# Performance work log

Hardware: AMD Instinct MI355X
Metric: run time of the kernel (lower is better)

Reference implementation:

```python
import jax, jax.numpy as jnp
import numpy as np
from jax import lax

B, C, L, G = 2048, 9605, 20, 50
ALPHA, ALPHA1, ALPHA2, ALPHA3, ALPHA_OTHER = 0.5, 0.05, 2.0, 10.0, 0.5
NEG_INF = jnp.float32(-1e30)


def setup_inputs() -> dict:
    k0, k1, k2, k3 = jax.random.split(jax.random.key(0), 4)
    x = jax.random.normal(k0, (B, C), jnp.float32)
    # sparse multi-label targets (~10 positives/row) so at most ~1 whitelist group is active,
    # matching the original code's assert len(gt_whitelist_index) == 1
    y = (jax.random.uniform(k1, (B, C)) < 0.001).astype(jnp.int32)
    y_neg = (jax.random.uniform(k2, (B, C)) < 0.001).astype(jnp.int32)
    # L disjoint whitelist groups of G classes each (from mapping_dict in the original)
    idx = jax.random.permutation(k3, C)[: L * G].reshape(L, G)
    group_mask = jnp.zeros((L, C), bool).at[jnp.arange(L)[:, None], idx].set(True)
    return {"x": x, "y": y, "y_neg": y_neg, "group_mask": group_mask}


def _rank_loss(x1, x2, margin):
    # our_rank_loss: sigmoid(alpha3*(x2-x1+margin)), scaled by alpha2 when positive
    d = x2 - x1 + margin
    s = jax.nn.sigmoid(ALPHA3 * d)
    return jnp.where(d > 0, ALPHA2 * s, s)


def reference(x, y, y_neg, group_mask):
    xs = jax.nn.sigmoid(x)  # [B, C]
    gmf = group_mask.astype(jnp.float32)  # [L, C]

    # per-row max score inside each whitelist group -> [B, L]
    # lax.map over the L (=20) groups keeps peak memory at one [B, C] temp per step
    group_max = lax.map(
        lambda m: jnp.max(jnp.where(m, xs, NEG_INF), axis=-1), group_mask
    ).T  # [B, L]

    # find_gt_whitelist: group k active iff sum(y[group_k]) > 0
    active = jnp.einsum("bc,lc->bl", y.astype(jnp.float32), gmf) > 0
    active_neg = jnp.einsum("bc,lc->bl", y_neg.astype(jnp.float32), gmf) > 0
    has_gt = jnp.any(active, axis=-1)  # [B]
    g = jnp.argmax(active, axis=-1)  # first active group (original asserts exactly one)

    # top_k_thres = max(11th largest sigmoid score, alpha_other) in both branches
    thres = jnp.maximum(lax.top_k(xs, 11)[0][:, 10], ALPHA_OTHER)  # [B]

    # max over union of all whitelist classes (wl_indices)
    union_max = jnp.max(jnp.where(jnp.any(group_mask, 0)[None, :], xs, NEG_INF), -1)

    gt_max = jnp.take_along_axis(group_max, g[:, None], axis=1)[:, 0]  # [B]
    # incorrect_max: max(0, max over groups != g); incorrect_neg: max(0, max over neg-active groups)
    excl = jnp.where(jnp.arange(L)[None, :] == g[:, None], NEG_INF, group_max)
    incorrect_max = jnp.maximum(jnp.max(excl, -1), 0.0)
    incorrect_neg = jnp.maximum(jnp.max(jnp.where(active_neg, group_max, 0.0), -1), 0.0)

    # branch A: no gt whitelist group active
    case_a = (1 - ALPHA) * _rank_loss(thres, union_max, ALPHA1) + ALPHA * _rank_loss(
        thres, incorrect_neg, ALPHA1
    )
    # branch B: exactly one gt group g
    case_b = (
        _rank_loss(gt_max, thres, ALPHA1)
        + jnp.where(
            incorrect_max > 0, (1 - ALPHA) * _rank_loss(thres, incorrect_max, ALPHA1), 0.0
        )
        + jnp.where(
            incorrect_neg > 0,
            ALPHA * _rank_loss(thres, incorrect_neg, ALPHA1),
            ALPHA * _rank_loss(thres, incorrect_max, ALPHA1),
        )
    )
    return jnp.sum(jnp.where(has_gt, case_b, case_a))
```

## Files before the change

kernel.cpp:

```cpp
#include <hip/hip_runtime.h>
#include <stdint.h>

#define B_ROWS 2048
#define C_CLS  9605
#define L_GRP  20
#define GM_BYTES (L_GRP * C_CLS)
#define REPSTRIDE 9728
#define GID_REGION (4 * REPSTRIDE)
#define NEG_BIG -3.0e38f

typedef float f32x4 __attribute__((ext_vector_type(4)));
typedef unsigned u32x4 __attribute__((ext_vector_type(4)));

__device__ __forceinline__ float sigmoidf(float v) {
  return 1.0f / (1.0f + __expf(-v));
}

__device__ __forceinline__ float rank_loss(float x1, float x2) {
  float d = x2 - x1 + 0.05f;
  float s = 1.0f / (1.0f + __expf(-10.0f * d));
  return d > 0.0f ? 2.0f * s : s;
}

__device__ __forceinline__ unsigned fmap(float f) {
  unsigned u = __float_as_uint(f);
  return (u & 0x80000000u) ? ~u : (u | 0x80000000u);
}
__device__ __forceinline__ float funmap(unsigned m) {
  unsigned u = (m & 0x80000000u) ? (m ^ 0x80000000u) : ~m;
  return __uint_as_float(u);
}

__global__ __launch_bounds__(256) void build_gid_kernel(
    const void* __restrict__ gm, unsigned char* __restrict__ ws,
    float* __restrict__ out) {
  __shared__ int s_part[4];
  __shared__ int s_total;
  const int tid = threadIdx.x;
  const int c = blockIdx.x * 256 + tid;
  if (c == 0) out[0] = 0.0f;

  int local = 0;
  const uint4* gm16 = (const uint4*)gm;
  const int nvec = GM_BYTES / 16;
  for (int i = tid; i < nvec; i += 256) {
    uint4 w = gm16[i];
    unsigned a[4] = {w.x, w.y, w.z, w.w};
#pragma unroll
    for (int q = 0; q < 4; ++q) {
      local += ((a[q] & 0x000000FFu) != 0) + ((a[q] & 0x0000FF00u) != 0) +
               ((a[q] & 0x00FF0000u) != 0) + ((a[q] & 0xFF000000u) != 0);
    }
  }
  if (tid == 0) {
    unsigned a = ((const unsigned*)gm)[nvec * 4];
    local += ((a & 0x000000FFu) != 0) + ((a & 0x0000FF00u) != 0) +
             ((a & 0x00FF0000u) != 0) + ((a & 0xFF000000u) != 0);
  }
#pragma unroll
  for (int off = 32; off; off >>= 1) local += __shfl_xor(local, off);
  if ((tid & 63) == 0) s_part[tid >> 6] = local;
  __syncthreads();
  if (tid == 0) s_total = s_part[0] + s_part[1] + s_part[2] + s_part[3];
  __syncthreads();
  const bool is_byte = (s_total > 600);

  if (c >= C_CLS) return;
  unsigned char g = 0xFF;
  if (is_byte) {
    const unsigned char* m8 = (const unsigned char*)gm;
#pragma unroll
    for (int l = L_GRP - 1; l >= 0; --l)
      if (m8[l * C_CLS + c] != 0) g = (unsigned char)l;
  } else {
    const unsigned* m32 = (const unsigned*)gm;
#pragma unroll
    for (int l = L_GRP - 1; l >= 0; --l)
      if (m32[l * C_CLS + c] != 0u) g = (unsigned char)l;
  }
  unsigned char* base = ws + 64;
#pragma unroll
  for (int r = 0; r < 4; ++r) base[r * REPSTRIDE + r + c] = g;
}

__global__ __launch_bounds__(256, 8) void loss_kernel(
    const float* __restrict__ x, const int* __restrict__ y,
    const int* __restrict__ yn, const unsigned char* __restrict__ ws64,
    float* __restrict__ out) {
  __shared__ unsigned s_gmax[L_GRP];
  __shared__ unsigned s_act, s_actn;
  __shared__ float s_wtop[4 * 11];
  const int tid = threadIdx.x;
  const int lane = tid & 63;
  const int wave = tid >> 6;
  const int row = blockIdx.x;

  const size_t base = (size_t)row * C_CLS;
  const int mis = (int)(base & 3);
  const int peel = (4 - mis) & 3;
  const float* xr = x + base;
  const int* yr = y + base;
  const int* nr = yn + base;
  const unsigned char* gidc = ws64 + mis * REPSTRIDE + mis;

  if (tid < L_GRP) s_gmax[tid] = 0u;
  if (tid == 0) { s_act = 0u; s_actn = 0u; }
  __syncthreads();

  float t[11];
#pragma unroll
  for (int i = 0; i < 11; ++i) t[i] = 0.0f;
  unsigned actL = 0u, actnL = 0u;

  auto ins = [&](float v) {
    if (v > t[10]) {
      float a = v;
#pragma unroll
      for (int i = 0; i < 11; ++i) {
        float hi = fmaxf(t[i], a); a = fminf(t[i], a); t[i] = hi;
      }
    }
  };
  auto gmax_upd = [&](unsigned gk, float v) {
    unsigned fm = fmap(v);
    if (fm > s_gmax[gk]) atomicMax(&s_gmax[gk], fm);
  };
  auto edge = [&](int c) {
    float v = xr[c];
    ins(v);
    unsigned gk = gidc[c];
    if (gk < L_GRP) {
      gmax_upd(gk, v);
      unsigned bit = 1u << gk;
      if (yr[c] != 0) actL |= bit;
      if (nr[c] != 0) actnL |= bit;
    }
  };

  if (tid < peel) edge(tid);
  const int nvec = (C_CLS - peel) >> 2;
  const int tail0 = peel + (nvec << 2);
  if (tid < C_CLS - tail0) edge(tail0 + tid);

  const f32x4* x4 = (const f32x4*)(xr + peel);
  const u32x4* y4 = (const u32x4*)(yr + peel);
  const u32x4* n4 = (const u32x4*)(nr + peel);
  const unsigned* g4 = (const unsigned*)(gidc + peel);

  auto quad = [&](f32x4 xv, u32x4 yv, u32x4 nv, unsigned gw) {
    if (gw != 0xFFFFFFFFu) {
      unsigned g0 = gw & 0xFFu, g1 = (gw >> 8) & 0xFFu,
               g2 = (gw >> 16) & 0xFFu, g3 = gw >> 24;
      if (g0 < L_GRP) gmax_upd(g0, xv.x);
      if (g1 < L_GRP) gmax_upd(g1, xv.y);
      if (g2 < L_GRP) gmax_upd(g2, xv.z);
      if (g3 < L_GRP) gmax_upd(g3, xv.w);
    }
    if (yv.x | yv.y | yv.z | yv.w | nv.x | nv.y | nv.z | nv.w) {
      const unsigned yq[4] = {yv.x, yv.y, yv.z, yv.w};
      const unsigned nq[4] = {nv.x, nv.y, nv.z, nv.w};
      const unsigned gq[4] = {gw & 0xFFu, (gw >> 8) & 0xFFu,
                              (gw >> 16) & 0xFFu, gw >> 24};
#pragma unroll
      for (int q = 0; q < 4; ++q) {
        if ((yq[q] | nq[q]) && gq[q] < L_GRP) {
          unsigned bit = 1u << gq[q];
          if (yq[q]) actL |= bit;
          if (nq[q]) actnL |= bit;
        }
      }
    }
    float am = fmaxf(fmaxf(xv.x, xv.y), fmaxf(xv.z, xv.w));
    if (am > t[10]) { ins(xv.x); ins(xv.y); ins(xv.z); ins(xv.w); }
  };

  int j = tid;
  for (; j + 256 < nvec; j += 512) {
    f32x4 xa = __builtin_nontemporal_load(x4 + j);
    f32x4 xb = __builtin_nontemporal_load(x4 + j + 256);
    u32x4 ya = __builtin_nontemporal_load(y4 + j);
    u32x4 yb = __builtin_nontemporal_load(y4 + j + 256);
    u32x4 na = __builtin_nontemporal_load(n4 + j);
    u32x4 nb = __builtin_nontemporal_load(n4 + j + 256);
    unsigned ga = g4[j];
    unsigned gb = g4[j + 256];
    quad(xa, ya, na, ga);
    quad(xb, yb, nb, gb);
  }
  for (; j < nvec; j += 256) {
    f32x4 xv = __builtin_nontemporal_load(x4 + j);
    u32x4 yv = __builtin_nontemporal_load(y4 + j);
    u32x4 nv = __builtin_nontemporal_load(n4 + j);
    quad(xv, yv, nv, g4[j]);
  }

  if (actL) atomicOr(&s_act, actL);
  if (actnL) atomicOr(&s_actn, actnL);

  float cur = t[0];
  float mr[11];
#pragma unroll
  for (int r = 0; r < 11; ++r) {
    float m = cur;
#pragma unroll
    for (int off = 32; off; off >>= 1) m = fmaxf(m, __shfl_xor(m, off));
    mr[r] = m;
    if (r < 10) {
      unsigned long long b = __ballot(cur == m);
      int leader = (int)(__ffsll(b) - 1);
      if (lane == leader) {
#pragma unroll
        for (int i = 0; i < 10; ++i) t[i] = t[i + 1];
        t[10] = NEG_BIG;
        cur = t[0];
      }
    }
  }
  if (lane == 0) {
#pragma unroll
    for (int r = 0; r < 11; ++r) s_wtop[wave * 11 + r] = mr[r];
  }
  __syncthreads();

  if (wave == 0) {
    float v = (lane < 44) ? s_wtop[lane] : NEG_BIG;
    float eleventh = NEG_BIG;
#pragma unroll
    for (int r = 0; r < 11; ++r) {
      float m = v;
#pragma unroll
      for (int off = 32; off; off >>= 1) m = fmaxf(m, __shfl_xor(m, off));
      eleventh = m;
      if (r < 10) {
        unsigned long long b = __ballot(v == m);
        int leader = (int)(__ffsll(b) - 1);
        if (lane == leader) v = NEG_BIG;
      }
    }

    const unsigned aL = s_act, anL = s_actn;
    const bool has_gt = (aL != 0u);
    const int g = has_gt ? (__ffs(aL) - 1) : 0;
    const float thres = fmaxf(sigmoidf(eleventh), 0.5f);

    float union_max = NEG_BIG, gt_sg = 0.0f, inc_max = NEG_BIG, inc_neg = 0.0f;
#pragma unroll
    for (int l = 0; l < L_GRP; ++l) {
      float sg = sigmoidf(funmap(s_gmax[l]));
      union_max = fmaxf(union_max, sg);
      if (l == g) gt_sg = sg; else inc_max = fmaxf(inc_max, sg);
      if ((anL >> l) & 1u) inc_neg = fmaxf(inc_neg, sg);
    }
    inc_max = fmaxf(inc_max, 0.0f);
    inc_neg = fmaxf(inc_neg, 0.0f);

    float loss;
    if (has_gt) {
      loss = rank_loss(gt_sg, thres);
      if (inc_max > 0.0f) loss += 0.5f * rank_loss(thres, inc_max);
      loss += 0.5f * rank_loss(thres, (inc_neg > 0.0f) ? inc_neg : inc_max);
    } else {
      loss = 0.5f * rank_loss(thres, union_max) + 0.5f * rank_loss(thres, inc_neg);
    }
    if (lane == 0) atomicAdd(out, loss);
  }
}

extern "C" void kernel_launch(void* const* d_in, const int* in_sizes, int n_in,
                              void* d_out, int out_size, void* d_ws, size_t ws_size,
                              hipStream_t stream) {
  (void)in_sizes; (void)n_in; (void)out_size; (void)ws_size;
  const float* x = (const float*)d_in[0];
  const int* y = (const int*)d_in[1];
  const int* yn = (const int*)d_in[2];
  const void* gm = d_in[3];

  unsigned char* ws = (unsigned char*)d_ws;
  unsigned char* ws64 = ws + 64;

  build_gid_kernel<<<(C_CLS + 255) / 256, 256, 0, stream>>>(gm, ws,
                                                            (float*)d_out);
  loss_kernel<<<B_ROWS, 256, 0, stream>>>(x, y, yn, ws64, (float*)d_out);
}
```

Measured before the change: 244.0 us.

## Split mask-type probe into grid-wide kernel and deepen loss load unroll

Result: faster. 234.9 us (median of 2 runs) (-3.7%).

```diff
diff --git a/kernel.cpp b/kernel.cpp
--- a/kernel.cpp
+++ b/kernel.cpp
@@ -7,6 +7,7 @@
 #define GM_BYTES (L_GRP * C_CLS)
 #define REPSTRIDE 9728
 #define GID_REGION (4 * REPSTRIDE)
+#define PCOUNT_OFF (64 + GID_REGION)
 #define NEG_BIG -3.0e38f
 
 typedef float f32x4 __attribute__((ext_vector_type(4)));
@@ -31,35 +32,50 @@
   return __uint_as_float(u);
 }
 
+__global__ __launch_bounds__(256) void probe_kernel(
+    const uint4* __restrict__ gm, float* __restrict__ out,
+    int* __restrict__ pcount) {
+  __shared__ int s_part[4];
+  const int tid = threadIdx.x;
+  const int bid = blockIdx.x;
+  const int gtid = bid * 256 + tid;
+  if (gtid == 0) out[0] = 0.0f;
+
+  int local = 0;
+  const int nvec = GM_BYTES / 16;
+  for (int i = gtid; i < nvec; i += 65536) {
+    uint4 w = gm[i];
+    unsigned a[4] = {w.x, w.y, w.z, w.w};
+#pragma unroll
+    for (int q = 0; q < 4; ++q) {
+      local += ((a[q] & 0x000000FFu) != 0) + ((a[q] & 0x0000FF00u) != 0) +
+               ((a[q] & 0x00FF0000u) != 0) + ((a[q] & 0xFF000000u) != 0);
+    }
+  }
+  if (gtid == nvec % 65536) {
+    unsigned a = ((const unsigned*)gm)[nvec * 4];
+    local += ((a & 0x000000FFu) != 0) + ((a & 0x0000FF00u) != 0) +
+             ((a & 0x00FF0000u) != 0) + ((a & 0xFF000000u) != 0);
+  }
+#pragma unroll
+  for (int off = 32; off; off >>= 1) local += __shfl_xor(local, off);
+  if ((tid & 63) == 0) s_part[tid >> 6] = local;
+  __syncthreads();
+  if (tid == 0) pcount[bid] = s_part[0] + s_part[1] + s_part[2] + s_part[3];
+}
+
 __global__ __launch_bounds__(256) void build_gid_kernel(
-    const void* __restrict__ gm, unsigned char* __restrict__ ws,
-    float* __restrict__ out) {
+    const void* __restrict__ gm, const int* __restrict__ pcount,
+    unsigned char* __restrict__ ws) {
   __shared__ int s_part[4];
   __shared__ int s_total;
   const int tid = threadIdx.x;
   const int c = blockIdx.x * 256 + tid;
-  if (c == 0) out[0] = 0.0f;
-
-  int local = 0;
-  const uint4* gm16 = (const uint4*)gm;
-  const int nvec = GM_BYTES / 16;
-  for (int i = tid; i < nvec; i += 256) {
-    uint4 w = gm16[i];
-    unsigned a[4] = {w.x, w.y, w.z, w.w};
-#pragma unroll
-    for (int q = 0; q < 4; ++q) {
-      local += ((a[q] & 0x000000FFu) != 0) + ((a[q] & 0x0000FF00u) != 0) +
-               ((a[q] & 0x00FF0000u) != 0) + ((a[q] & 0xFF000000u) != 0);
-    }
-  }
-  if (tid == 0) {
-    unsigned a = ((const unsigned*)gm)[nvec * 4];
-    local += ((a & 0x000000FFu) != 0) + ((a & 0x0000FF00u) != 0) +
-             ((a & 0x00FF0000u) != 0) + ((a & 0xFF000000u) != 0);
-  }
-#pragma unroll
-  for (int off = 32; off; off >>= 1) local += __shfl_xor(local, off);
-  if ((tid & 63) == 0) s_part[tid >> 6] = local;
+
+  int v = pcount[tid];
+#pragma unroll
+  for (int off = 32; off; off >>= 1) v += __shfl_xor(v, off);
+  if ((tid & 63) == 0) s_part[tid >> 6] = v;
   __syncthreads();
   if (tid == 0) s_total = s_part[0] + s_part[1] + s_part[2] + s_part[3];
   __syncthreads();
@@ -83,7 +99,7 @@
   for (int r = 0; r < 4; ++r) base[r * REPSTRIDE + r + c] = g;
 }
 
-__global__ __launch_bounds__(256, 8) void loss_kernel(
+__global__ __launch_bounds__(256, 4) void loss_kernel(
     const float* __restrict__ x, const int* __restrict__ y,
     const int* __restrict__ yn, const unsigned char* __restrict__ ws64,
     float* __restrict__ out) {
@@ -175,17 +191,27 @@
   };
 
   int j = tid;
-  for (; j + 256 < nvec; j += 512) {
+  for (; j + 768 < nvec; j += 1024) {
     f32x4 xa = __builtin_nontemporal_load(x4 + j);
     f32x4 xb = __builtin_nontemporal_load(x4 + j + 256);
+    f32x4 xc = __builtin_nontemporal_load(x4 + j + 512);
+    f32x4 xd = __builtin_nontemporal_load(x4 + j + 768);
     u32x4 ya = __builtin_nontemporal_load(y4 + j);
     u32x4 yb = __builtin_nontemporal_load(y4 + j + 256);
+    u32x4 yc = __builtin_nontemporal_load(y4 + j + 512);
+    u32x4 yd = __builtin_nontemporal_load(y4 + j + 768);
     u32x4 na = __builtin_nontemporal_load(n4 + j);
     u32x4 nb = __builtin_nontemporal_load(n4 + j + 256);
+    u32x4 nc = __builtin_nontemporal_load(n4 + j + 512);
+    u32x4 nd = __builtin_nontemporal_load(n4 + j + 768);
     unsigned ga = g4[j];
     unsigned gb = g4[j + 256];
+    unsigned gc = g4[j + 512];
+    unsigned gd = g4[j + 768];
     quad(xa, ya, na, ga);
     quad(xb, yb, nb, gb);
+    quad(xc, yc, nc, gc);
+    quad(xd, yd, nd, gd);
   }
   for (; j < nvec; j += 256) {
     f32x4 xv = __builtin_nontemporal_load(x4 + j);
@@ -277,8 +303,10 @@
 
   unsigned char* ws = (unsigned char*)d_ws;
   unsigned char* ws64 = ws + 64;
-
-  build_gid_kernel<<<(C_CLS + 255) / 256, 256, 0, stream>>>(gm, ws,
-                                                            (float*)d_out);
+  int* pcount = (int*)(ws + PCOUNT_OFF);
+
+  probe_kernel<<<256, 256, 0, stream>>>((const uint4*)gm, (float*)d_out,
+                                        pcount);
+  build_gid_kernel<<<(C_CLS + 255) / 256, 256, 0, stream>>>(gm, pcount, ws);
   loss_kernel<<<B_ROWS, 256, 0, stream>>>(x, y, yn, ws64, (float*)d_out);
 }
```
